# Kernel tuning notes

Measured on AMD Instinct MI355X. Metric: run time of the kernel, lower is better.

## Reference

```python
import jax, jax.numpy as jnp
import numpy as np

NUM_HEADS = 16

def setup_inputs() -> dict:
    key = jax.random.key(0)
    ks = jax.random.split(key, 7)
    B, Q, K, D = 4, 512, 4096, 1024
    return {
        'query':  jax.random.normal(ks[0], (B, Q, D), dtype=jnp.float32),
        'memory': jax.random.normal(ks[1], (B, K, D), dtype=jnp.float32),
        'bias':   jax.random.normal(ks[2], (B, K), dtype=jnp.float32),
        'Wq': jax.random.normal(ks[3], (D, D), dtype=jnp.float32) * (D ** -0.5),
        'Wk': jax.random.normal(ks[4], (D, D), dtype=jnp.float32) * (D ** -0.5),
        'Wv': jax.random.normal(ks[5], (D, D), dtype=jnp.float32) * (D ** -0.5),
        'Wo': jax.random.normal(ks[6], (D, D), dtype=jnp.float32) * (D ** -0.5),
    }

def reference(query, memory, bias, Wq, Wk, Wv, Wo):
    B, Qn, _ = query.shape
    _, Kn, _ = memory.shape
    H = NUM_HEADS
    E = Wq.shape[1]
    dh = E // H
    scale = dh ** -0.5
    # projections (bias-free linears), split heads: [B, H, len, dh]
    q = (query @ Wq).reshape(B, Qn, H, dh).transpose(0, 2, 1, 3)
    k = (memory @ Wk).reshape(B, Kn, H, dh).transpose(0, 2, 1, 3)
    v = (memory @ Wv).reshape(B, Kn, H, dh).transpose(0, 2, 1, 3)
    scores = jnp.einsum('bhqd,bhkd->bhqk', q, k) * scale
    scores = scores + bias[:, None, None, :]          # additive support bias over K
    weights = jax.nn.softmax(scores, axis=-1)          # dropout p=0.0 -> identity
    out = jnp.einsum('bhqk,bhkd->bhqd', weights, v)
    out = out.transpose(0, 2, 1, 3).reshape(B, Qn, E)
    return out @ Wo
```

## Files before the change

kernel.cpp:

```cpp
#include <hip/hip_runtime.h>

typedef __attribute__((ext_vector_type(8))) short bf16x8;
typedef __attribute__((ext_vector_type(4))) short bf16x4;
typedef __attribute__((ext_vector_type(4))) float f32x4;

#define MFMA32(a,b,c) __builtin_amdgcn_mfma_f32_16x16x32_bf16((a),(b),(c),0,0,0)
#define MFMA16(a,b,c) __builtin_amdgcn_mfma_f32_16x16x16bf16_1k((a),(b),(c),0,0,0)
#define LOG2E 1.44269504f

__device__ __forceinline__ unsigned short f2bf(float f) {
  unsigned int u = __float_as_uint(f);
  u += 0x7fffu + ((u >> 16) & 1u);
  return (unsigned short)(u >> 16);
}

__device__ __forceinline__ void cp16(const void* g, void* l) {
  __builtin_amdgcn_global_load_lds((const __attribute__((address_space(1))) void*)g,
                                   (__attribute__((address_space(3))) void*)l, 16, 0, 0);
}

__global__ void conv_both(const float* __restrict__ q, const float* __restrict__ m,
                          const float* __restrict__ bias,
                          unsigned short* __restrict__ qo, unsigned short* __restrict__ mo,
                          float* __restrict__ bz) {
  int i = blockIdx.x * 256 + threadIdx.x;
  if (i < 524288) {
    float4 v = ((const float4*)q)[i];
    ushort4 o; o.x = f2bf(v.x); o.y = f2bf(v.y); o.z = f2bf(v.z); o.w = f2bf(v.w);
    ((ushort4*)qo)[i] = o;
  } else if (i < 4718592) {
    int j = i - 524288;
    float4 v = ((const float4*)m)[j];
    ushort4 o; o.x = f2bf(v.x); o.y = f2bf(v.y); o.z = f2bf(v.z); o.w = f2bf(v.w);
    ((ushort4*)mo)[j] = o;
  } else {
    int j = i - 4718592;
    float4 v = ((const float4*)bias)[j];
    float4 o;
    o.x = __builtin_fmaf(v.x, LOG2E, -16.f);
    o.y = __builtin_fmaf(v.y, LOG2E, -16.f);
    o.z = __builtin_fmaf(v.z, LOG2E, -16.f);
    o.w = __builtin_fmaf(v.w, LOG2E, -16.f);
    ((float4*)bz)[j] = o;
  }
}

__global__ void transpose4(const float* __restrict__ Wq, const float* __restrict__ Wk,
                           const float* __restrict__ Wv, const float* __restrict__ Wo,
                           unsigned short* __restrict__ dst) {
  __shared__ float t[32][33];
  int z = blockIdx.z;
  const float* W = (z == 0) ? Wq : (z == 1) ? Wk : (z == 2) ? Wv : Wo;
  unsigned short* WT = dst + (size_t)z * 1048576;
  int bx = blockIdx.x * 32, by = blockIdx.y * 32;
  int x = threadIdx.x, y0 = threadIdx.y;
#pragma unroll
  for (int r = 0; r < 4; ++r)
    t[y0 + r * 8][x] = W[(size_t)(by + y0 + r * 8) * 1024 + bx + x];
  __syncthreads();
#pragma unroll
  for (int r = 0; r < 4; ++r)
    WT[(size_t)(bx + y0 + r * 8) * 1024 + by + x] = f2bf(t[x][y0 + r * 8]);
}

__global__ __launch_bounds__(256, 2) void gemm_kv(
    const unsigned short* __restrict__ A,
    const unsigned short* __restrict__ Bk,
    const unsigned short* __restrict__ Bv,
    unsigned short* __restrict__ Kp,
    unsigned short* __restrict__ Vt)
{
  __shared__ __attribute__((aligned(16))) unsigned short lds[12288];
  int w = threadIdx.x >> 6, lane = threadIdx.x & 63;
  int lh = lane & 15, q4 = lane >> 4;
  int id = blockIdx.x;
  int xcd = id & 7, j = id >> 3;
  int tm = (xcd * 16 + (j >> 3)) * 128;
  int tn = (j & 7) * 128;
  int wm = (w & 1) * 64, wn = (w >> 1) * 64;

  f32x4 acck[4][4] = {}, accv[4][4] = {};

  for (int k0 = 0; k0 < 1024; k0 += 32) {
#pragma unroll
    for (int i = 0; i < 2; ++i) {
      int c = w * 2 + i;
      int o = c * 1024 + lane * 16;
      int row = o >> 6, colu = (o & 63) >> 1;
      cp16(A  + (size_t)(tm + row) * 1024 + k0 + colu, lds + c * 512);
      cp16(Bk + (size_t)(tn + row) * 1024 + k0 + colu, lds + 4096 + c * 512);
      cp16(Bv + (size_t)(tn + row) * 1024 + k0 + colu, lds + 8192 + c * 512);
    }
    __syncthreads();
    bf16x8 afr[4], bkf[4], bvf[4];
#pragma unroll
    for (int r = 0; r < 4; ++r)
      afr[r] = *(const bf16x8*)(lds + (wm + r * 16 + lh) * 32 + q4 * 8);
#pragma unroll
    for (int c = 0; c < 4; ++c) {
      bkf[c] = *(const bf16x8*)(lds + 4096 + (wn + c * 16 + lh) * 32 + q4 * 8);
      bvf[c] = *(const bf16x8*)(lds + 8192 + (wn + c * 16 + lh) * 32 + q4 * 8);
    }
#pragma unroll
    for (int r = 0; r < 4; ++r)
#pragma unroll
      for (int c = 0; c < 4; ++c) {
        acck[r][c] = MFMA32(afr[r], bkf[c], acck[r][c]);
        accv[r][c] = MFMA32(afr[r], bvf[c], accv[r][c]);
      }
    __syncthreads();
  }

#pragma unroll
  for (int r = 0; r < 4; ++r)
#pragma unroll
    for (int c = 0; c < 4; ++c) {
      int row = tm + wm + r * 16 + q4 * 4;
      int col = tn + wn + c * 16 + lh;
#pragma unroll
      for (int e = 0; e < 4; ++e)
        Kp[(size_t)(row + e) * 1024 + col] = f2bf(acck[r][c][e]);
      ushort4 v4;
      v4.x = f2bf(accv[r][c][0]); v4.y = f2bf(accv[r][c][1]);
      v4.z = f2bf(accv[r][c][2]); v4.w = f2bf(accv[r][c][3]);
      *(ushort4*)(Vt + (size_t)col * 16384 + row) = v4;
    }
}

__global__ __launch_bounds__(256) void gemm_bt64(
    const unsigned short* __restrict__ A, const unsigned short* __restrict__ B,
    float* __restrict__ Cf, unsigned short* __restrict__ Cb,
    int M, int N, int K, float scale)
{
  __shared__ __attribute__((aligned(16))) unsigned short lds[6144];
  int w = threadIdx.x >> 6, lane = threadIdx.x & 63;
  int lh = lane & 15, q4 = lane >> 4;
  int tm = blockIdx.y * 128, tn = blockIdx.x * 64;
  int wm = (w & 1) * 64, wn = (w >> 1) * 32;

  f32x4 acc[4][2] = {};

  for (int k0 = 0; k0 < K; k0 += 32) {
#pragma unroll
    for (int i = 0; i < 2; ++i) {
      int c = w * 2 + i;
      int o = c * 1024 + lane * 16;
      int row = o >> 6, colu = (o & 63) >> 1;
      cp16(A + (size_t)(tm + row) * K + k0 + colu, lds + c * 512);
    }
    {
      int o = w * 1024 + lane * 16;
      int row = o >> 6, colu = (o & 63) >> 1;
      cp16(B + (size_t)(tn + row) * K + k0 + colu, lds + 4096 + w * 512);
    }
    __syncthreads();
    bf16x8 afr[4], bfr[2];
#pragma unroll
    for (int r = 0; r < 4; ++r)
      afr[r] = *(const bf16x8*)(lds + (wm + r * 16 + lh) * 32 + q4 * 8);
#pragma unroll
    for (int c = 0; c < 2; ++c)
      bfr[c] = *(const bf16x8*)(lds + 4096 + (wn + c * 16 + lh) * 32 + q4 * 8);
#pragma unroll
    for (int r = 0; r < 4; ++r)
#pragma unroll
      for (int c = 0; c < 2; ++c)
        acc[r][c] = MFMA32(afr[r], bfr[c], acc[r][c]);
    __syncthreads();
  }

#pragma unroll
  for (int r = 0; r < 4; ++r)
#pragma unroll
    for (int c = 0; c < 2; ++c)
#pragma unroll
      for (int e = 0; e < 4; ++e) {
        int row = tm + wm + r * 16 + q4 * 4 + e;
        int col = tn + wn + c * 16 + lh;
        if (Cb) Cb[(size_t)row * N + col] = f2bf(acc[r][c][e] * scale);
        else    Cf[(size_t)row * N + col] = acc[r][c][e] * scale;
      }
}

__global__ __launch_bounds__(256) void attn_kernel(
    const unsigned short* __restrict__ Q, const unsigned short* __restrict__ Kp,
    const unsigned short* __restrict__ VT, const float* __restrict__ bz,
    float* __restrict__ po, float* __restrict__ lp)
{
  __shared__ __attribute__((aligned(16))) unsigned short Klds[4096];
  __shared__ __attribute__((aligned(16))) unsigned short Vlds[4096];
  int w = threadIdx.x >> 6, lane = threadIdx.x & 63;
  int lh = lane & 15, q4 = lane >> 4;

  int id = blockIdx.x;
  int xcd = id & 7, j = id >> 3;
  int ql = j & 7;
  int half = ql & 1, qt = ql >> 1;
  int bh = (j >> 3) * 8 + xcd;
  int b = bh >> 4, h = bh & 15;
  int q0 = qt * 128;
  int t00 = half * 2048;

  const unsigned short* Qb = Q + (size_t)(b * 512 + q0 + w * 32) * 1024 + h * 64;
  const unsigned short* Kb = Kp + (size_t)(b * 4096) * 1024 + h * 64;
  const unsigned short* Vb = VT + (size_t)(h * 64) * 16384 + b * 4096;
  const float* bzg = bz + (size_t)b * 4096;

  bf16x8 bq[2][2];
#pragma unroll
  for (int s = 0; s < 2; ++s)
#pragma unroll
    for (int th = 0; th < 2; ++th)
      bq[s][th] = *(const bf16x8*)(Qb + (size_t)(s * 16 + lh) * 1024 + th * 32 + q4 * 8);

  f32x4 oa[2][4] = {};
  float ls[2] = {0.f, 0.f};

  int rl = lane >> 3, blk = lane & 7;
  int sw = ((blk ^ rl) * 8);

  for (int ti = 0; ti < 32; ++ti) {
    int t = t00 + ti * 64;
#pragma unroll
    for (int r = 0; r < 2; ++r) {
      int seg = r * 4 + w;
      int row = seg * 8 + rl;
      cp16(Kb + (size_t)(t + row) * 1024 + sw, Klds + seg * 512);
      cp16(Vb + (size_t)row * 16384 + t + sw, Vlds + seg * 512);
    }
    __syncthreads();

    float4 bz4[4];
#pragma unroll
    for (int c = 0; c < 4; ++c)
      bz4[c] = *(const float4*)(bzg + t + c * 16 + q4 * 4);

    bf16x8 kf[4][2];
#pragma unroll
    for (int c = 0; c < 4; ++c)
#pragma unroll
      for (int th = 0; th < 2; ++th)
        kf[c][th] = *(const bf16x8*)(Klds + (c * 16 + lh) * 64 + (((th << 2) + q4) ^ (lh & 7)) * 8);
    bf16x4 vf[4][4];
#pragma unroll
    for (int c = 0; c < 4; ++c)
#pragma unroll
      for (int c2 = 0; c2 < 4; ++c2)
        vf[c][c2] = *(const bf16x4*)(Vlds + (c2 * 16 + lh) * 64 +
                                     (((c << 1) + (q4 >> 1)) ^ (lh & 7)) * 8 + (q4 & 1) * 4);

#pragma unroll
    for (int s = 0; s < 2; ++s) {
#pragma unroll
      for (int c = 0; c < 4; ++c) {
        f32x4 z = {};
        z = MFMA32(kf[c][0], bq[s][0], z);
        z = MFMA32(kf[c][1], bq[s][1], z);
        float bzf[4] = {bz4[c].x, bz4[c].y, bz4[c].z, bz4[c].w};
        bf16x4 pb;
        float ps = 0.f;
#pragma unroll
        for (int e = 0; e < 4; ++e) {
          float p = __builtin_amdgcn_exp2f(z[e] + bzf[e]);
          ps += p;
          pb[e] = (short)f2bf(p);
        }
        ls[s] += ps;
#pragma unroll
        for (int c2 = 0; c2 < 4; ++c2)
          oa[s][c2] = MFMA16(vf[c][c2], pb, oa[s][c2]);
      }
    }
    __syncthreads();
  }

#pragma unroll
  for (int s = 0; s < 2; ++s) {
    ls[s] += __shfl_xor(ls[s], 16);
    ls[s] += __shfl_xor(ls[s], 32);
  }

  int sl = bh * 4 + qt;
  float* pslice = po + (size_t)(half * 256 + sl) * 8192;
#pragma unroll
  for (int s = 0; s < 2; ++s) {
    if (q4 == 0) lp[half * 32768 + sl * 128 + w * 32 + s * 16 + lh] = ls[s];
#pragma unroll
    for (int c2 = 0; c2 < 4; ++c2)
#pragma unroll
      for (int e = 0; e < 4; ++e)
        pslice[(c2 * 16 + q4 * 4 + e) * 128 + w * 32 + s * 16 + lh] = oa[s][c2][e];
  }
}

__global__ void norm_kernel(const float* __restrict__ po, const float* __restrict__ lp,
                            unsigned short* __restrict__ ao) {
  int g = blockIdx.x * 256 + threadIdx.x;
  int d8 = (g & 7) * 8;
  int rowid = g >> 3;
  int bh = rowid >> 9, rq = rowid & 511, qt = rq >> 7, qcol = rq & 127;
  int sl = bh * 4 + qt;
  const float* p0 = po + (size_t)sl * 8192;
  const float* p1 = po + (size_t)(256 + sl) * 8192;
  float l = lp[sl * 128 + qcol] + lp[32768 + sl * 128 + qcol];
  float inv = 1.f / l;
  unsigned short o8[8];
#pragma unroll
  for (int k = 0; k < 8; ++k)
    o8[k] = f2bf((p0[(d8 + k) * 128 + qcol] + p1[(d8 + k) * 128 + qcol]) * inv);
  int b = bh >> 4, h = bh & 15;
  unsigned short* dst = ao + (size_t)(b * 512 + qt * 128 + qcol) * 1024 + h * 64 + d8;
  *(ushort4*)dst = *(ushort4*)o8;
  *(ushort4*)(dst + 4) = *(ushort4*)(o8 + 4);
}

extern "C" void kernel_launch(void* const* d_in, const int* in_sizes, int n_in,
                              void* d_out, int out_size, void* d_ws, size_t ws_size,
                              hipStream_t stream) {
  const float* query  = (const float*)d_in[0];
  const float* memory = (const float*)d_in[1];
  const float* bias   = (const float*)d_in[2];
  const float* Wq     = (const float*)d_in[3];
  const float* Wk     = (const float*)d_in[4];
  const float* Wv     = (const float*)d_in[5];
  const float* Wo     = (const float*)d_in[6];
  float* out = (float*)d_out;

  unsigned short* ws  = (unsigned short*)d_ws;
  unsigned short* qbf = ws;
  unsigned short* mbf = qbf + 2097152;
  unsigned short* WqT = mbf + 16777216;
  unsigned short* WkT = WqT + 1048576;
  unsigned short* WvT = WkT + 1048576;
  unsigned short* WoT = WvT + 1048576;
  unsigned short* qp  = WoT + 1048576;
  unsigned short* kp  = qp + 2097152;
  unsigned short* vT  = kp + 16777216;
  unsigned short* ao  = vT + 16777216;
  float* bzw = (float*)(ao + 2097152);
  float* po = (float*)ws;
  float* lp = po + 4194304;

  conv_both<<<18448, 256, 0, stream>>>(query, memory, bias, qbf, mbf, bzw);
  transpose4<<<dim3(32, 32, 4), dim3(32, 8), 0, stream>>>(Wq, Wk, Wv, Wo, WqT);

  gemm_bt64<<<dim3(16, 16), 256, 0, stream>>>(qbf, WqT, nullptr, qp, 2048, 1024, 1024, 0.125f * LOG2E);
  gemm_kv<<<1024, 256, 0, stream>>>(mbf, WkT, WvT, kp, vT);

  attn_kernel<<<512, 256, 0, stream>>>(qp, kp, vT, bzw, po, lp);
  norm_kernel<<<1024, 256, 0, stream>>>(po, lp, ao);

  gemm_bt64<<<dim3(16, 16), 256, 0, stream>>>(ao, WoT, out, nullptr, 2048, 1024, 1024, 1.f);
}
```

Measured before the change: 309.3 us.

## Double-buffer attention tiles, k-major LDS layout, smaller GEMM tiles

The attention kernel now runs with 2 waves per block, each owning 64 query rows. One wave loads K and the other loads V^T, into double-buffered LDS with a k-major (column-chunk) layout, so the next tile's loads overlap the current tile's compute. gemm_kv and the projection GEMM switch to the same k-major LDS layout to cut bank conflicts on fragment reads. The projection GEMM moves to 64x64 tiles with twice as many blocks, giving more parallelism but less reuse per block. Halving the threads per attention block doubles the register accumulators per wave and may lower occupancy.

```diff
diff --git a/kernel.cpp b/kernel.cpp
--- a/kernel.cpp
+++ b/kernel.cpp
@@ -84,22 +84,21 @@
   for (int k0 = 0; k0 < 1024; k0 += 32) {
 #pragma unroll
     for (int i = 0; i < 2; ++i) {
-      int c = w * 2 + i;
-      int o = c * 1024 + lane * 16;
-      int row = o >> 6, colu = (o & 63) >> 1;
-      cp16(A  + (size_t)(tm + row) * 1024 + k0 + colu, lds + c * 512);
-      cp16(Bk + (size_t)(tn + row) * 1024 + k0 + colu, lds + 4096 + c * 512);
-      cp16(Bv + (size_t)(tn + row) * 1024 + k0 + colu, lds + 8192 + c * 512);
+      int s = w * 2 + i;
+      int p = s >> 1, rh = s & 1;
+      cp16(A  + (size_t)(tm + rh * 64 + lane) * 1024 + k0 + p * 8, lds + s * 512);
+      cp16(Bk + (size_t)(tn + rh * 64 + lane) * 1024 + k0 + p * 8, lds + 4096 + s * 512);
+      cp16(Bv + (size_t)(tn + rh * 64 + lane) * 1024 + k0 + p * 8, lds + 8192 + s * 512);
     }
     __syncthreads();
     bf16x8 afr[4], bkf[4], bvf[4];
 #pragma unroll
     for (int r = 0; r < 4; ++r)
-      afr[r] = *(const bf16x8*)(lds + (wm + r * 16 + lh) * 32 + q4 * 8);
+      afr[r] = *(const bf16x8*)(lds + q4 * 1024 + (wm + r * 16 + lh) * 8);
 #pragma unroll
     for (int c = 0; c < 4; ++c) {
-      bkf[c] = *(const bf16x8*)(lds + 4096 + (wn + c * 16 + lh) * 32 + q4 * 8);
-      bvf[c] = *(const bf16x8*)(lds + 8192 + (wn + c * 16 + lh) * 32 + q4 * 8);
+      bkf[c] = *(const bf16x8*)(lds + 4096 + q4 * 1024 + (wn + c * 16 + lh) * 8);
+      bvf[c] = *(const bf16x8*)(lds + 8192 + q4 * 1024 + (wn + c * 16 + lh) * 8);
     }
 #pragma unroll
     for (int r = 0; r < 4; ++r)
@@ -127,42 +126,32 @@
     }
 }
 
-__global__ __launch_bounds__(256) void gemm_bt64(
+__global__ __launch_bounds__(256) void gemm64(
     const unsigned short* __restrict__ A, const unsigned short* __restrict__ B,
     float* __restrict__ Cf, unsigned short* __restrict__ Cb,
     int M, int N, int K, float scale)
 {
-  __shared__ __attribute__((aligned(16))) unsigned short lds[6144];
+  __shared__ __attribute__((aligned(16))) unsigned short lds[4096];
   int w = threadIdx.x >> 6, lane = threadIdx.x & 63;
   int lh = lane & 15, q4 = lane >> 4;
-  int tm = blockIdx.y * 128, tn = blockIdx.x * 64;
-  int wm = (w & 1) * 64, wn = (w >> 1) * 32;
-
-  f32x4 acc[4][2] = {};
+  int tm = blockIdx.y * 64, tn = blockIdx.x * 64;
+  int wm = (w & 1) * 32, wn = (w >> 1) * 32;
+
+  f32x4 acc[2][2] = {};
 
   for (int k0 = 0; k0 < K; k0 += 32) {
-#pragma unroll
-    for (int i = 0; i < 2; ++i) {
-      int c = w * 2 + i;
-      int o = c * 1024 + lane * 16;
-      int row = o >> 6, colu = (o & 63) >> 1;
-      cp16(A + (size_t)(tm + row) * K + k0 + colu, lds + c * 512);
-    }
-    {
-      int o = w * 1024 + lane * 16;
-      int row = o >> 6, colu = (o & 63) >> 1;
-      cp16(B + (size_t)(tn + row) * K + k0 + colu, lds + 4096 + w * 512);
-    }
-    __syncthreads();
-    bf16x8 afr[4], bfr[2];
-#pragma unroll
-    for (int r = 0; r < 4; ++r)
-      afr[r] = *(const bf16x8*)(lds + (wm + r * 16 + lh) * 32 + q4 * 8);
+    cp16(A + (size_t)(tm + lane) * K + k0 + w * 8, lds + w * 512);
+    cp16(B + (size_t)(tn + lane) * K + k0 + w * 8, lds + 2048 + w * 512);
+    __syncthreads();
+    bf16x8 afr[2], bfr[2];
+#pragma unroll
+    for (int r = 0; r < 2; ++r)
+      afr[r] = *(const bf16x8*)(lds + q4 * 512 + (wm + r * 16 + lh) * 8);
 #pragma unroll
     for (int c = 0; c < 2; ++c)
-      bfr[c] = *(const bf16x8*)(lds + 4096 + (wn + c * 16 + lh) * 32 + q4 * 8);
-#pragma unroll
-    for (int r = 0; r < 4; ++r)
+      bfr[c] = *(const bf16x8*)(lds + 2048 + q4 * 512 + (wn + c * 16 + lh) * 8);
+#pragma unroll
+    for (int r = 0; r < 2; ++r)
 #pragma unroll
       for (int c = 0; c < 2; ++c)
         acc[r][c] = MFMA32(afr[r], bfr[c], acc[r][c]);
@@ -170,7 +159,7 @@
   }
 
 #pragma unroll
-  for (int r = 0; r < 4; ++r)
+  for (int r = 0; r < 2; ++r)
 #pragma unroll
     for (int c = 0; c < 2; ++c)
 #pragma unroll
@@ -182,13 +171,12 @@
       }
 }
 
-__global__ __launch_bounds__(256) void attn_kernel(
+__global__ __launch_bounds__(128) void attn_kernel(
     const unsigned short* __restrict__ Q, const unsigned short* __restrict__ Kp,
     const unsigned short* __restrict__ VT, const float* __restrict__ bz,
     float* __restrict__ po, float* __restrict__ lp)
 {
-  __shared__ __attribute__((aligned(16))) unsigned short Klds[4096];
-  __shared__ __attribute__((aligned(16))) unsigned short Vlds[4096];
+  __shared__ __attribute__((aligned(16))) unsigned short lds[16384];
   int w = threadIdx.x >> 6, lane = threadIdx.x & 63;
   int lh = lane & 15, q4 = lane >> 4;
 
@@ -201,62 +189,66 @@
   int q0 = qt * 128;
   int t00 = half * 2048;
 
-  const unsigned short* Qb = Q + (size_t)(b * 512 + q0 + w * 32) * 1024 + h * 64;
+  const unsigned short* Qb = Q + (size_t)(b * 512 + q0 + w * 64) * 1024 + h * 64;
   const unsigned short* Kb = Kp + (size_t)(b * 4096) * 1024 + h * 64;
   const unsigned short* Vb = VT + (size_t)(h * 64) * 16384 + b * 4096;
   const float* bzg = bz + (size_t)b * 4096;
 
-  bf16x8 bq[2][2];
-#pragma unroll
-  for (int s = 0; s < 2; ++s)
+  bf16x8 bq[4][2];
+#pragma unroll
+  for (int s = 0; s < 4; ++s)
 #pragma unroll
     for (int th = 0; th < 2; ++th)
       bq[s][th] = *(const bf16x8*)(Qb + (size_t)(s * 16 + lh) * 1024 + th * 32 + q4 * 8);
 
-  f32x4 oa[2][4] = {};
-  float ls[2] = {0.f, 0.f};
-
-  int rl = lane >> 3, blk = lane & 7;
-  int sw = ((blk ^ rl) * 8);
+  f32x4 oa[4][4] = {};
+  float ls[4] = {0.f, 0.f, 0.f, 0.f};
+
+  if (w == 0) {
+#pragma unroll
+    for (int s = 0; s < 8; ++s)
+      cp16(Kb + (size_t)(t00 + lane) * 1024 + s * 8, lds + s * 512);
+  } else {
+#pragma unroll
+    for (int s = 0; s < 8; ++s)
+      cp16(Vb + (size_t)lane * 16384 + t00 + s * 8, lds + 4096 + s * 512);
+  }
 
   for (int ti = 0; ti < 32; ++ti) {
+    __syncthreads();
+    int cur = (ti & 1) * 8192;
+    if (ti + 1 < 32) {
+      int tn_ = t00 + (ti + 1) * 64;
+      int nxt = ((ti + 1) & 1) * 8192;
+      if (w == 0) {
+#pragma unroll
+        for (int s = 0; s < 8; ++s)
+          cp16(Kb + (size_t)(tn_ + lane) * 1024 + s * 8, lds + nxt + s * 512);
+      } else {
+#pragma unroll
+        for (int s = 0; s < 8; ++s)
+          cp16(Vb + (size_t)lane * 16384 + tn_ + s * 8, lds + nxt + 4096 + s * 512);
+      }
+    }
     int t = t00 + ti * 64;
-#pragma unroll
-    for (int r = 0; r < 2; ++r) {
-      int seg = r * 4 + w;
-      int row = seg * 8 + rl;
-      cp16(Kb + (size_t)(t + row) * 1024 + sw, Klds + seg * 512);
-      cp16(Vb + (size_t)row * 16384 + t + sw, Vlds + seg * 512);
-    }
-    __syncthreads();
-
-    float4 bz4[4];
-#pragma unroll
-    for (int c = 0; c < 4; ++c)
-      bz4[c] = *(const float4*)(bzg + t + c * 16 + q4 * 4);
-
-    bf16x8 kf[4][2];
-#pragma unroll
-    for (int c = 0; c < 4; ++c)
-#pragma unroll
-      for (int th = 0; th < 2; ++th)
-        kf[c][th] = *(const bf16x8*)(Klds + (c * 16 + lh) * 64 + (((th << 2) + q4) ^ (lh & 7)) * 8);
-    bf16x4 vf[4][4];
-#pragma unroll
-    for (int c = 0; c < 4; ++c)
+    const unsigned short* Kl = lds + cur;
+    const unsigned short* Vl = lds + cur + 4096;
+
+#pragma unroll
+    for (int c = 0; c < 4; ++c) {
+      bf16x8 kf0 = *(const bf16x8*)(Kl + (q4) * 512 + (c * 16 + lh) * 8);
+      bf16x8 kf1 = *(const bf16x8*)(Kl + (4 + q4) * 512 + (c * 16 + lh) * 8);
+      bf16x4 vf[4];
 #pragma unroll
       for (int c2 = 0; c2 < 4; ++c2)
-        vf[c][c2] = *(const bf16x4*)(Vlds + (c2 * 16 + lh) * 64 +
-                                     (((c << 1) + (q4 >> 1)) ^ (lh & 7)) * 8 + (q4 & 1) * 4);
-
-#pragma unroll
-    for (int s = 0; s < 2; ++s) {
-#pragma unroll
-      for (int c = 0; c < 4; ++c) {
+        vf[c2] = *(const bf16x4*)(Vl + (c * 2 + (q4 >> 1)) * 512 + (c2 * 16 + lh) * 8 + (q4 & 1) * 4);
+      float4 b4 = *(const float4*)(bzg + t + c * 16 + q4 * 4);
+      float bzf[4] = {b4.x, b4.y, b4.z, b4.w};
+#pragma unroll
+      for (int s = 0; s < 4; ++s) {
         f32x4 z = {};
-        z = MFMA32(kf[c][0], bq[s][0], z);
-        z = MFMA32(kf[c][1], bq[s][1], z);
-        float bzf[4] = {bz4[c].x, bz4[c].y, bz4[c].z, bz4[c].w};
+        z = MFMA32(kf0, bq[s][0], z);
+        z = MFMA32(kf1, bq[s][1], z);
         bf16x4 pb;
         float ps = 0.f;
 #pragma unroll
@@ -268,14 +260,13 @@
         ls[s] += ps;
 #pragma unroll
         for (int c2 = 0; c2 < 4; ++c2)
-          oa[s][c2] = MFMA16(vf[c][c2], pb, oa[s][c2]);
+          oa[s][c2] = MFMA16(vf[c2], pb, oa[s][c2]);
       }
     }
-    __syncthreads();
-  }
-
-#pragma unroll
-  for (int s = 0; s < 2; ++s) {
+  }
+
+#pragma unroll
+  for (int s = 0; s < 4; ++s) {
     ls[s] += __shfl_xor(ls[s], 16);
     ls[s] += __shfl_xor(ls[s], 32);
   }
@@ -283,13 +274,13 @@
   int sl = bh * 4 + qt;
   float* pslice = po + (size_t)(half * 256 + sl) * 8192;
 #pragma unroll
-  for (int s = 0; s < 2; ++s) {
-    if (q4 == 0) lp[half * 32768 + sl * 128 + w * 32 + s * 16 + lh] = ls[s];
+  for (int s = 0; s < 4; ++s) {
+    if (q4 == 0) lp[half * 32768 + sl * 128 + w * 64 + s * 16 + lh] = ls[s];
 #pragma unroll
     for (int c2 = 0; c2 < 4; ++c2)
 #pragma unroll
       for (int e = 0; e < 4; ++e)
-        pslice[(c2 * 16 + q4 * 4 + e) * 128 + w * 32 + s * 16 + lh] = oa[s][c2][e];
+        pslice[(c2 * 16 + q4 * 4 + e) * 128 + w * 64 + s * 16 + lh] = oa[s][c2][e];
   }
 }
 
@@ -344,11 +335,11 @@
   conv_both<<<18448, 256, 0, stream>>>(query, memory, bias, qbf, mbf, bzw);
   transpose4<<<dim3(32, 32, 4), dim3(32, 8), 0, stream>>>(Wq, Wk, Wv, Wo, WqT);
 
-  gemm_bt64<<<dim3(16, 16), 256, 0, stream>>>(qbf, WqT, nullptr, qp, 2048, 1024, 1024, 0.125f * LOG2E);
+  gemm64<<<dim3(16, 32), 256, 0, stream>>>(qbf, WqT, nullptr, qp, 2048, 1024, 1024, 0.125f * LOG2E);
   gemm_kv<<<1024, 256, 0, stream>>>(mbf, WkT, WvT, kp, vT);
 
-  attn_kernel<<<512, 256, 0, stream>>>(qp, kp, vT, bzw, po, lp);
+  attn_kernel<<<512, 128, 0, stream>>>(qp, kp, vT, bzw, po, lp);
   norm_kernel<<<1024, 256, 0, stream>>>(po, lp, ao);
 
-  gemm_bt64<<<dim3(16, 16), 256, 0, stream>>>(ao, WoT, out, nullptr, 2048, 1024, 1024, 1.f);
-}
+  gemm64<<<dim3(16, 32), 256, 0, stream>>>(ao, WoT, out, nullptr, 2048, 1024, 1024, 1.f);
+}
```

After: 386.9 us. +25.1%, slower.
